# Performance work log

Hardware: AMD Instinct MI355X
Metric: run time of the kernel (lower is better)

## Reference

```python
import jax, jax.numpy as jnp
import numpy as np

BN_EPS = 1e-5
DIST_EPS = 1e-8


def setup_inputs() -> dict:
    key = jax.random.key(0)
    ks = jax.random.split(key, 8)
    B, N, S, D1, D2 = 8, 16384, 2048, 128, 256
    return {
        "xyz1": jax.random.normal(ks[0], (B, N, 3), jnp.float32),
        "xyz2": jax.random.normal(ks[1], (B, S, 3), jnp.float32),
        "points1": jax.random.normal(ks[2], (B, N, D1), jnp.float32),
        "points2": jax.random.normal(ks[3], (B, S, D2), jnp.float32),
        "w1": jax.random.normal(ks[4], (256, 384), jnp.float32) * 0.05,
        "b1": jnp.zeros((256,), jnp.float32),
        "g1": jnp.ones((256,), jnp.float32),
        "be1": jnp.zeros((256,), jnp.float32),
        "w2": jax.random.normal(ks[5], (128, 256), jnp.float32) * 0.05,
        "b2": jnp.zeros((128,), jnp.float32),
        "g2": jnp.ones((128,), jnp.float32),
        "be2": jnp.zeros((128,), jnp.float32),
        "fa1": jax.random.normal(ks[6], (16, 128), jnp.float32) * 0.1,
        "fa2": jax.random.normal(ks[7], (128, 16), jnp.float32) * 0.1,
    }


def _three_interp(xyz1, xyz2, points2):
    # squared pairwise distance [B,N,S]
    d = (jnp.sum(xyz1 ** 2, -1)[:, :, None]
         + jnp.sum(xyz2 ** 2, -1)[:, None, :]
         - 2.0 * jnp.einsum("bnc,bsc->bns", xyz1, xyz2))
    neg_d, idx = jax.lax.top_k(-d, 3)          # 3 smallest distances
    dist = -neg_d                               # [B,N,3]
    recip = 1.0 / (dist + DIST_EPS)
    w = recip / jnp.sum(recip, -1, keepdims=True)
    B, N, _ = idx.shape
    D = points2.shape[-1]
    gathered = jnp.take_along_axis(
        points2, idx.reshape(B, N * 3)[..., None], axis=1
    ).reshape(B, N, 3, D)
    return jnp.sum(gathered * w[..., None], axis=-2)  # [B,N,D]


def _bn_relu(h, g, be):
    # train-mode BatchNorm1d: stats over (batch, length)
    mu = jnp.mean(h, axis=(0, 1))
    var = jnp.var(h, axis=(0, 1))
    return jax.nn.relu(g * (h - mu) / jnp.sqrt(var + BN_EPS) + be)


def reference(xyz1, xyz2, points1, points2, w1, b1, g1, be1,
              w2, b2, g2, be2, fa1, fa2):
    interp = _three_interp(xyz1, xyz2, points2)          # [B,N,256]
    x = jnp.concatenate([points1, interp], axis=-1)      # [B,N,384]
    # 1x1 Conv1d + BN + ReLU stack (channel-last)
    x = _bn_relu(jnp.einsum("bnc,oc->bno", x, w1) + b1, g1, be1)  # [B,N,256]
    x = _bn_relu(jnp.einsum("bnc,oc->bno", x, w2) + b2, g2, be2)  # [B,N,128]
    # channel attention (SE-style, avg + max pool over length)
    def fc(v):  # v: [B,C]
        return jax.nn.relu(v @ fa1.T) @ fa2.T
    avg = jnp.mean(x, axis=1)
    mx = jnp.max(x, axis=1)
    scale = jax.nn.sigmoid(fc(avg) + fc(mx))             # [B,C]
    return x * scale[:, None, :]                          # [B,N,128]
```

## Files before the change

kernel.cpp:

```cpp
#include <hip/hip_runtime.h>
#include <math.h>

constexpr int BB = 8;
constexpr int NN = 16384;
constexpr int SS = 2048;
constexpr int D2 = 256;
constexpr int H1 = 256;
constexpr int H2 = 128;
constexpr int MM = BB * NN;
constexpr int LDB = 40;

typedef __attribute__((ext_vector_type(8))) short short8;
typedef __attribute__((ext_vector_type(16))) float f32x16;

__device__ __forceinline__ unsigned short f2b(float f) {
    union { float f; unsigned u; } v; v.f = f;
    unsigned r = v.u + 0x7FFFu + ((v.u >> 16) & 1u);
    return (unsigned short)(r >> 16);
}
__device__ __forceinline__ unsigned pk2(float lo, float hi) {
    return (unsigned)f2b(lo) | ((unsigned)f2b(hi) << 16);
}
__device__ __forceinline__ float b2f_lo(unsigned p) { return __uint_as_float(p << 16); }
__device__ __forceinline__ float b2f_hi(unsigned p) { return __uint_as_float(p & 0xFFFF0000u); }

__global__ void k_init(float* __restrict__ st1, float* __restrict__ st2,
                       float* __restrict__ psum, int* __restrict__ pmax) {
    int t = threadIdx.x;
    if (t < 512) st1[t] = 0.f;
    if (t < 256) st2[t] = 0.f;
    if (t < 1024) { psum[t] = 0.f; pmax[t] = 0; }
}

__global__ void k_wprep(const float* __restrict__ w1, const float* __restrict__ w2,
                        unsigned short* __restrict__ w1b, unsigned short* __restrict__ w2b) {
    int i = blockIdx.x * 256 + threadIdx.x;
    if (i < H1 * 384) w1b[i] = f2b(w1[i]);
    if (i < H2 * 256) w2b[i] = f2b(w2[i]);
}

__global__ void k_xyzprep(const float* __restrict__ xyz2, float4* __restrict__ xyz2p) {
    int i = blockIdx.x * 256 + threadIdx.x;
    if (i < BB * SS) {
        xyz2p[i] = make_float4(xyz2[i * 3], xyz2[i * 3 + 1], xyz2[i * 3 + 2], 0.f);
    }
}

__global__ __launch_bounds__(256) void k_knn(const float* __restrict__ xyz1,
                                             const float4* __restrict__ xyz2p,
                                             int* __restrict__ idx,
                                             float* __restrict__ wgt) {
    __shared__ unsigned cand[64][16];
    const int b = blockIdx.y;
    const int tid = threadIdx.x;
    const int ql = tid & 63;
    const int n = blockIdx.x * 64 + ql;

    const float* q = xyz1 + ((size_t)b * NN + n) * 3;
    const float qx = q[0], qy = q[1], qz = q[2];

    const int chunk = __builtin_amdgcn_readfirstlane(tid >> 6);
    const float4* cp = xyz2p + ((size_t)b << 11) + (chunk << 9);

    unsigned k0 = 0xFFFFFFFFu, k1 = 0xFFFFFFFFu, k2 = 0xFFFFFFFFu, k3 = 0xFFFFFFFFu;
#pragma unroll 4
    for (int j = 0; j < 512; ++j) {
        const float4 p = cp[j];
        const float dx = qx - p.x;
        const float dy = qy - p.y;
        const float dz = qz - p.z;
        const float d = fmaf(dx, dx, fmaf(dy, dy, dz * dz));
        const unsigned key = (__float_as_uint(d) & 0xFFFFFE00u) | (unsigned)j;
        unsigned m;
        m  = max(k0, key); k0 = min(k0, key);
        unsigned m2 = max(k1, m); k1 = min(k1, m);
        unsigned m3 = max(k2, m2); k2 = min(k2, m2);
        k3 = min(k3, m3);
    }
    unsigned* cq = cand[ql] + chunk * 4;
    cq[0] = k0; cq[1] = k1; cq[2] = k2; cq[3] = k3;
    __syncthreads();

    if (tid < 64) {
        const double qxd = (double)qx, qyd = (double)qy, qzd = (double)qz;
        double t0 = 1e300, t1 = 1e300, t2 = 1e300;
        int i0 = 0, i1 = 0, i2 = 0;
#pragma unroll
        for (int c = 0; c < 16; ++c) {
            const int s = ((c >> 2) << 9) + (int)(cand[tid][c] & 0x1FFu);
            const float4 p = xyz2p[((size_t)b << 11) + s];
            const double dx = qxd - (double)p.x;
            const double dy = qyd - (double)p.y;
            const double dz = qzd - (double)p.z;
            const double d = fma(dx, dx, fma(dy, dy, dz * dz));
            if (d < t2) {
                if (d < t0)      { t2 = t1; i2 = i1; t1 = t0; i1 = i0; t0 = d; i0 = s; }
                else if (d < t1) { t2 = t1; i2 = i1; t1 = d; i1 = s; }
                else             { t2 = d; i2 = s; }
            }
        }
        const double r0 = 1.0 / (t0 + 1e-8);
        const double r1 = 1.0 / (t1 + 1e-8);
        const double r2 = 1.0 / (t2 + 1e-8);
        const double inv = 1.0 / (r0 + r1 + r2);
        const size_t o = ((size_t)b * NN + n) * 3;
        idx[o + 0] = i0; idx[o + 1] = i1; idx[o + 2] = i2;
        wgt[o + 0] = (float)(r0 * inv);
        wgt[o + 1] = (float)(r1 * inv);
        wgt[o + 2] = (float)(r2 * inv);
    }
}

__global__ __launch_bounds__(256, 2) void k_gemm1(const float* __restrict__ p1,
                                                  const float* __restrict__ p2,
                                                  const int* __restrict__ idx,
                                                  const float* __restrict__ wgt,
                                                  const unsigned short* __restrict__ w1b,
                                                  const float* __restrict__ b1p,
                                                  unsigned short* __restrict__ h1b,
                                                  float* __restrict__ st1) {
    __shared__ __align__(16) unsigned short As[128 * LDB];
    __shared__ __align__(16) unsigned short Bs[256 * LDB];
    __shared__ float sSum[256], sSq[256];

    const int tid = threadIdx.x;
    const int row0 = blockIdx.x * 128;
    const int b = row0 >> 14;
    const float* p2b = p2 + (size_t)b * (SS * D2);

    sSum[tid] = 0.f; sSq[tid] = 0.f;

    const int wave = tid >> 6, lane = tid & 63;
    const int ln = lane & 31, hk = lane >> 5;
    const int wm = (wave & 1) << 6;
    const int wn = (wave >> 1) << 7;
    const int r = tid >> 1, half = tid & 1;

    const size_t o3 = (size_t)(row0 + r) * 3;
    const int j0 = idx[o3], j1 = idx[o3 + 1], j2 = idx[o3 + 2];
    const float wa = wgt[o3], wb = wgt[o3 + 1], wc = wgt[o3 + 2];
    const float* g0 = p2b + ((size_t)j0 << 8);
    const float* g1 = p2b + ((size_t)j1 << 8);
    const float* g2 = p2b + ((size_t)j2 << 8);

    f32x16 acc[2][4];
#pragma unroll
    for (int mt = 0; mt < 2; ++mt)
#pragma unroll
        for (int nt = 0; nt < 4; ++nt)
#pragma unroll
            for (int e = 0; e < 16; ++e) acc[mt][nt][e] = 0.f;

    float4 ra[12];
    uint4 rb[4];

    auto prefetch = [&](int kc) {
        const unsigned short* bsrc = w1b + (size_t)tid * 384 + kc * 32;
        rb[0] = *(const uint4*)(bsrc);
        rb[1] = *(const uint4*)(bsrc + 8);
        rb[2] = *(const uint4*)(bsrc + 16);
        rb[3] = *(const uint4*)(bsrc + 24);
        if (kc < 4) {
            const float* src = p1 + (((size_t)(row0 + r)) << 7) + kc * 32 + half * 16;
            ra[0] = *(const float4*)(src);
            ra[1] = *(const float4*)(src + 4);
            ra[2] = *(const float4*)(src + 8);
            ra[3] = *(const float4*)(src + 12);
        } else {
            const int c2 = kc * 32 - 128 + half * 16;
#pragma unroll
            for (int g = 0; g < 4; ++g) {
                ra[g]     = *(const float4*)(g0 + c2 + g * 4);
                ra[4 + g] = *(const float4*)(g1 + c2 + g * 4);
                ra[8 + g] = *(const float4*)(g2 + c2 + g * 4);
            }
        }
    };

    prefetch(0);

    for (int kc = 0; kc < 12; ++kc) {
        uint4 pa0, pa1;
        if (kc < 4) {
            pa0 = make_uint4(pk2(ra[0].x, ra[0].y), pk2(ra[0].z, ra[0].w),
                             pk2(ra[1].x, ra[1].y), pk2(ra[1].z, ra[1].w));
            pa1 = make_uint4(pk2(ra[2].x, ra[2].y), pk2(ra[2].z, ra[2].w),
                             pk2(ra[3].x, ra[3].y), pk2(ra[3].z, ra[3].w));
        } else {
            float v[16];
#pragma unroll
            for (int g = 0; g < 4; ++g) {
                v[g * 4 + 0] = fmaf(wa, ra[g].x, fmaf(wb, ra[4 + g].x, wc * ra[8 + g].x));
                v[g * 4 + 1] = fmaf(wa, ra[g].y, fmaf(wb, ra[4 + g].y, wc * ra[8 + g].y));
                v[g * 4 + 2] = fmaf(wa, ra[g].z, fmaf(wb, ra[4 + g].z, wc * ra[8 + g].z));
                v[g * 4 + 3] = fmaf(wa, ra[g].w, fmaf(wb, ra[4 + g].w, wc * ra[8 + g].w));
            }
            pa0 = make_uint4(pk2(v[0], v[1]), pk2(v[2], v[3]), pk2(v[4], v[5]), pk2(v[6], v[7]));
            pa1 = make_uint4(pk2(v[8], v[9]), pk2(v[10], v[11]), pk2(v[12], v[13]), pk2(v[14], v[15]));
        }
        const uint4 wb0 = rb[0], wb1 = rb[1], wb2 = rb[2], wb3 = rb[3];

        __syncthreads();
        *(uint4*)&As[r * LDB + half * 16] = pa0;
        *(uint4*)&As[r * LDB + half * 16 + 8] = pa1;
        *(uint4*)&Bs[tid * LDB + 0]  = wb0;
        *(uint4*)&Bs[tid * LDB + 8]  = wb1;
        *(uint4*)&Bs[tid * LDB + 16] = wb2;
        *(uint4*)&Bs[tid * LDB + 24] = wb3;
        __syncthreads();

        if (kc < 11) prefetch(kc + 1);

        short8 af[2][2], bfv[4][2];
#pragma unroll
        for (int mt = 0; mt < 2; ++mt)
#pragma unroll
            for (int ks = 0; ks < 2; ++ks)
                af[mt][ks] = *(const short8*)&As[(wm + mt * 32 + ln) * LDB + ks * 16 + hk * 8];
#pragma unroll
        for (int nt = 0; nt < 4; ++nt)
#pragma unroll
            for (int ks = 0; ks < 2; ++ks)
                bfv[nt][ks] = *(const short8*)&Bs[(wn + nt * 32 + ln) * LDB + ks * 16 + hk * 8];
#pragma unroll
        for (int mt = 0; mt < 2; ++mt)
#pragma unroll
            for (int nt = 0; nt < 4; ++nt)
#pragma unroll
                for (int ks = 0; ks < 2; ++ks)
                    acc[mt][nt] = __builtin_amdgcn_mfma_f32_32x32x16_bf16(
                        af[mt][ks], bfv[nt][ks], acc[mt][nt], 0, 0, 0);
    }

#pragma unroll
    for (int nt = 0; nt < 4; ++nt) {
        const int col = wn + nt * 32 + ln;
        const float bias = b1p[col];
        float ps = 0.f, pq = 0.f;
#pragma unroll
        for (int mt = 0; mt < 2; ++mt) {
#pragma unroll
            for (int e = 0; e < 16; ++e) {
                const int rl = wm + mt * 32 + (e & 3) + ((e >> 2) << 3) + (hk << 2);
                const float o = acc[mt][nt][e] + bias;
                ps += o;
                pq = fmaf(o, o, pq);
                h1b[(((size_t)(row0 + rl)) << 8) + col] = f2b(o);
            }
        }
        atomicAdd(&sSum[col], ps);
        atomicAdd(&sSq[col], pq);
    }
    __syncthreads();
    atomicAdd(&st1[tid], sSum[tid]);
    atomicAdd(&st1[256 + tid], sSq[tid]);
}

__global__ void k_bnprep(const float* __restrict__ st, const float* __restrict__ g,
                         const float* __restrict__ be, float* __restrict__ bn,
                         int C, float invM) {
    int c = blockIdx.x * blockDim.x + threadIdx.x;
    if (c < C) {
        float mean = st[c] * invM;
        float var = st[C + c] * invM - mean * mean;
        float a = g[c] / sqrtf(var + 1e-5f);
        bn[c] = a;
        bn[C + c] = fmaf(-mean, a, be[c]);
    }
}

__global__ __launch_bounds__(256) void k_gemm2(const unsigned short* __restrict__ h1b,
                                               const unsigned short* __restrict__ w2b,
                                               const float* __restrict__ b2p,
                                               const float* __restrict__ bn1,
                                               unsigned short* __restrict__ h2b,
                                               float* __restrict__ st2) {
    __shared__ __align__(16) unsigned short As[128 * LDB];
    __shared__ __align__(16) unsigned short Bs[128 * LDB];
    __shared__ float sBNa[256], sBNb[256];
    __shared__ float sSum[128], sSq[128];

    const int tid = threadIdx.x;
    const int row0 = blockIdx.x * 128;

    sBNa[tid] = bn1[tid];
    sBNb[tid] = bn1[256 + tid];
    if (tid < 128) { sSum[tid] = 0.f; sSq[tid] = 0.f; }

    const int wave = tid >> 6, lane = tid & 63;
    const int ln = lane & 31, hk = lane >> 5;
    const int wm = (wave & 1) << 6, wn = (wave >> 1) << 6;
    const int r = tid >> 1, half = tid & 1;

    f32x16 acc[2][2];
#pragma unroll
    for (int mt = 0; mt < 2; ++mt)
#pragma unroll
        for (int nt = 0; nt < 2; ++nt)
#pragma unroll
            for (int e = 0; e < 16; ++e) acc[mt][nt][e] = 0.f;

    uint4 rA0, rA1, rB0, rB1;
    auto prefetch = [&](int kc) {
        const unsigned short* asrc = h1b + (size_t)(row0 + r) * 256 + kc * 32 + half * 16;
        rA0 = *(const uint4*)asrc;
        rA1 = *(const uint4*)(asrc + 8);
        const unsigned short* bsrc = w2b + (size_t)r * 256 + kc * 32 + half * 16;
        rB0 = *(const uint4*)bsrc;
        rB1 = *(const uint4*)(bsrc + 8);
    };

    prefetch(0);
    __syncthreads();

    for (int kc = 0; kc < 8; ++kc) {
        const int k0 = kc * 32 + half * 16;
        unsigned pw[8] = {rA0.x, rA0.y, rA0.z, rA0.w, rA1.x, rA1.y, rA1.z, rA1.w};
        unsigned po[8];
#pragma unroll
        for (int gi = 0; gi < 8; ++gi) {
            float lo = b2f_lo(pw[gi]);
            float hi = b2f_hi(pw[gi]);
            lo = fmaxf(fmaf(sBNa[k0 + 2 * gi], lo, sBNb[k0 + 2 * gi]), 0.f);
            hi = fmaxf(fmaf(sBNa[k0 + 2 * gi + 1], hi, sBNb[k0 + 2 * gi + 1]), 0.f);
            po[gi] = pk2(lo, hi);
        }
        const uint4 pa0 = make_uint4(po[0], po[1], po[2], po[3]);
        const uint4 pa1 = make_uint4(po[4], po[5], po[6], po[7]);
        const uint4 qb0 = rB0, qb1 = rB1;

        __syncthreads();
        *(uint4*)&As[r * LDB + half * 16] = pa0;
        *(uint4*)&As[r * LDB + half * 16 + 8] = pa1;
        *(uint4*)&Bs[r * LDB + half * 16] = qb0;
        *(uint4*)&Bs[r * LDB + half * 16 + 8] = qb1;
        __syncthreads();

        if (kc < 7) prefetch(kc + 1);

        short8 af[2][2], bfv[2][2];
#pragma unroll
        for (int mt = 0; mt < 2; ++mt)
#pragma unroll
            for (int ks = 0; ks < 2; ++ks)
                af[mt][ks] = *(const short8*)&As[(wm + mt * 32 + ln) * LDB + ks * 16 + hk * 8];
#pragma unroll
        for (int nt = 0; nt < 2; ++nt)
#pragma unroll
            for (int ks = 0; ks < 2; ++ks)
                bfv[nt][ks] = *(const short8*)&Bs[(wn + nt * 32 + ln) * LDB + ks * 16 + hk * 8];
#pragma unroll
        for (int mt = 0; mt < 2; ++mt)
#pragma unroll
            for (int nt = 0; nt < 2; ++nt)
#pragma unroll
                for (int ks = 0; ks < 2; ++ks)
                    acc[mt][nt] = __builtin_amdgcn_mfma_f32_32x32x16_bf16(
                        af[mt][ks], bfv[nt][ks], acc[mt][nt], 0, 0, 0);
    }

#pragma unroll
    for (int nt = 0; nt < 2; ++nt) {
        const int col = wn + nt * 32 + ln;
        const float bias = b2p[col];
        float ps = 0.f, pq = 0.f;
#pragma unroll
        for (int mt = 0; mt < 2; ++mt) {
#pragma unroll
            for (int e = 0; e < 16; ++e) {
                const int rl = wm + mt * 32 + (e & 3) + ((e >> 2) << 3) + (hk << 2);
                const float o = acc[mt][nt][e] + bias;
                ps += o;
                pq = fmaf(o, o, pq);
                h2b[(((size_t)(row0 + rl)) << 7) + col] = f2b(o);
            }
        }
        atomicAdd(&sSum[col], ps);
        atomicAdd(&sSq[col], pq);
    }
    __syncthreads();
    if (tid < 128) {
        atomicAdd(&st2[tid], sSum[tid]);
        atomicAdd(&st2[128 + tid], sSq[tid]);
    }
}

__global__ __launch_bounds__(256) void k_pool(const unsigned short* __restrict__ h2b,
                                              const float* __restrict__ bn2,
                                              float* __restrict__ psum,
                                              int* __restrict__ pmax) {
    const int b = blockIdx.y;
    const int n0 = blockIdx.x * 256;
    const int tid = threadIdx.x;
    const int c = tid & 127, rh = tid >> 7;
    const float a = bn2[c], bc = bn2[128 + c];
    const unsigned short* base = h2b + (((size_t)b * NN + n0 + rh) << 7) + c;
    float s = 0.f, m = 0.f;
    for (int i = 0; i < 128; ++i) {
        float v = __uint_as_float((unsigned)base[(size_t)i * 256] << 16);
        float x = fmaxf(fmaf(a, v, bc), 0.f);
        s += x;
        m = fmaxf(m, x);
    }
    __shared__ float rs[256];
    __shared__ float rm[256];
    rs[tid] = s; rm[tid] = m;
    __syncthreads();
    if (tid < 128) {
        float ts = rs[tid] + rs[tid + 128];
        float tm = fmaxf(rm[tid], rm[tid + 128]);
        atomicAdd(&psum[b * 128 + c], ts);
        atomicMax(&pmax[b * 128 + c], __float_as_int(tm));
    }
}

__global__ __launch_bounds__(1024) void k_attn(const float* __restrict__ psum,
                                               const int* __restrict__ pmax,
                                               const float* __restrict__ fa1,
                                               const float* __restrict__ fa2,
                                               const float* __restrict__ bn2,
                                               float* __restrict__ sa,
                                               float* __restrict__ sb) {
    __shared__ float tS[128];
    const int tid = threadIdx.x;
    if (tid < 128) {
        const int b = tid >> 4, j = tid & 15;
        float da = 0.f, dm = 0.f;
        for (int cc = 0; cc < 128; ++cc) {
            float f = fa1[j * 128 + cc];
            da = fmaf(psum[b * 128 + cc] * (1.0f / 16384.0f), f, da);
            dm = fmaf(__int_as_float(pmax[b * 128 + cc]), f, dm);
        }
        tS[tid] = fmaxf(da, 0.f) + fmaxf(dm, 0.f);
    }
    __syncthreads();
    const int b = tid >> 7, c = tid & 127;
    float s = 0.f;
#pragma unroll
    for (int j = 0; j < 16; ++j) s = fmaf(tS[b * 16 + j], fa2[c * 16 + j], s);
    const float sc = 1.f / (1.f + expf(-s));
    sa[b * 128 + c] = bn2[c] * sc;
    sb[b * 128 + c] = bn2[128 + c] * sc;
}

__global__ void k_final(const unsigned short* __restrict__ h2b, const float* __restrict__ sa,
                        const float* __restrict__ sb, float* __restrict__ out) {
    const size_t i = (size_t)blockIdx.x * blockDim.x + threadIdx.x;
    const int cg = (int)(i & 15) * 8;
    const size_t row = i >> 4;
    const int b = (int)(row >> 14);
    const uint4 h = *(const uint4*)(h2b + (row << 7) + cg);
    const float4 A0 = *(const float4*)&sa[b * 128 + cg];
    const float4 A1 = *(const float4*)&sa[b * 128 + cg + 4];
    const float4 B0 = *(const float4*)&sb[b * 128 + cg];
    const float4 B1 = *(const float4*)&sb[b * 128 + cg + 4];
    float4 o0, o1;
    o0.x = fmaxf(fmaf(A0.x, b2f_lo(h.x), B0.x), 0.f);
    o0.y = fmaxf(fmaf(A0.y, b2f_hi(h.x), B0.y), 0.f);
    o0.z = fmaxf(fmaf(A0.z, b2f_lo(h.y), B0.z), 0.f);
    o0.w = fmaxf(fmaf(A0.w, b2f_hi(h.y), B0.w), 0.f);
    o1.x = fmaxf(fmaf(A1.x, b2f_lo(h.z), B1.x), 0.f);
    o1.y = fmaxf(fmaf(A1.y, b2f_hi(h.z), B1.y), 0.f);
    o1.z = fmaxf(fmaf(A1.z, b2f_lo(h.w), B1.z), 0.f);
    o1.w = fmaxf(fmaf(A1.w, b2f_hi(h.w), B1.w), 0.f);
    *(float4*)(out + (row << 7) + cg) = o0;
    *(float4*)(out + (row << 7) + cg + 4) = o1;
}

extern "C" void kernel_launch(void* const* d_in, const int* in_sizes, int n_in,
                              void* d_out, int out_size, void* d_ws, size_t ws_size,
                              hipStream_t stream) {
    const float* xyz1 = (const float*)d_in[0];
    const float* xyz2 = (const float*)d_in[1];
    const float* p1   = (const float*)d_in[2];
    const float* p2   = (const float*)d_in[3];
    const float* w1   = (const float*)d_in[4];
    const float* b1   = (const float*)d_in[5];
    const float* g1   = (const float*)d_in[6];
    const float* be1  = (const float*)d_in[7];
    const float* w2   = (const float*)d_in[8];
    const float* b2   = (const float*)d_in[9];
    const float* g2   = (const float*)d_in[10];
    const float* be2  = (const float*)d_in[11];
    const float* fa1  = (const float*)d_in[12];
    const float* fa2  = (const float*)d_in[13];
    float* out = (float*)d_out;

    char* ws = (char*)d_ws;
    int*   idx  = (int*)ws;
    float* wgt  = (float*)(ws + 1572864);
    unsigned short* h1b = (unsigned short*)(ws + 3145728);
    unsigned short* h2b = (unsigned short*)(ws + 70254592);
    float* st1  = (float*)(ws + 103809024);
    float* bn1  = st1 + 512;
    float* st2  = bn1 + 512;
    float* bn2  = st2 + 256;
    float* psum = bn2 + 256;
    int*   pmax = (int*)(psum + 1024);
    float* sa   = (float*)(pmax + 1024);
    float* sb   = sa + 1024;
    unsigned short* w1b = (unsigned short*)(sb + 1024);
    unsigned short* w2b = w1b + 98304;
    float4* xyz2p = (float4*)(ws + 104857600);

    k_init<<<1, 1024, 0, stream>>>(st1, st2, psum, pmax);
    k_wprep<<<(H1 * 384 + 255) / 256, 256, 0, stream>>>(w1, w2, w1b, w2b);
    k_xyzprep<<<(BB * SS + 255) / 256, 256, 0, stream>>>(xyz2, xyz2p);
    k_knn<<<dim3(NN / 64, BB), 256, 0, stream>>>(xyz1, xyz2p, idx, wgt);
    k_gemm1<<<MM / 128, 256, 0, stream>>>(p1, p2, idx, wgt, w1b, b1, h1b, st1);
    k_bnprep<<<1, 256, 0, stream>>>(st1, g1, be1, bn1, 256, 1.0f / (float)MM);
    k_gemm2<<<MM / 128, 256, 0, stream>>>(h1b, w2b, b2, bn1, h2b, st2);
    k_bnprep<<<1, 128, 0, stream>>>(st2, g2, be2, bn2, 128, 1.0f / (float)MM);
    k_pool<<<dim3(NN / 256, BB), 256, 0, stream>>>(h2b, bn2, psum, pmax);
    k_attn<<<1, 1024, 0, stream>>>(psum, pmax, fa1, fa2, bn2, sa, sb);
    k_final<<<(MM * H2 / 8) / 256, 256, 0, stream>>>(h2b, sa, sb, out);
}
```

Before: 413.9 us.

## Precompute points2 projection through W1 and interpolate projected features

Since the interpolation is linear, the points2 part of the first conv is computed once per source point (Z = points2·W1[:,128:]) in a new small GEMM kernel. The main GEMM then covers only the 128 points1 channels and adds a weighted gather of three Z rows in its epilogue. This cuts the interpolated GEMM work and gather traffic roughly by the N/S ratio. In exchange, the epilogue does scattered fp32 gathers from an 16 MB Z buffer that reuses the h2b workspace. Tiles shrink to 64 rows so occupancy is raised to 3 blocks.

```diff
diff --git a/kernel.cpp b/kernel.cpp
--- a/kernel.cpp
+++ b/kernel.cpp
@@ -111,146 +111,204 @@
     }
 }
 
-__global__ __launch_bounds__(256, 2) void k_gemm1(const float* __restrict__ p1,
-                                                  const float* __restrict__ p2,
+__global__ __launch_bounds__(256) void k_zprep(const float* __restrict__ p2,
+                                               const unsigned short* __restrict__ w1b,
+                                               float* __restrict__ Z) {
+    __shared__ __align__(16) unsigned short As[64 * LDB];
+    __shared__ __align__(16) unsigned short Bs[256 * LDB];
+    const int tid = threadIdx.x;
+    const int s0 = blockIdx.x * 64;
+    const int wave = tid >> 6, lane = tid & 63;
+    const int ln = lane & 31, hk = lane >> 5;
+    const int wn = wave << 6;
+    const int r = tid >> 2, q = tid & 3;
+
+    f32x16 acc[2][2];
+#pragma unroll
+    for (int mt = 0; mt < 2; ++mt)
+#pragma unroll
+        for (int nt = 0; nt < 2; ++nt)
+#pragma unroll
+            for (int e = 0; e < 16; ++e) acc[mt][nt][e] = 0.f;
+
+    float4 ra[2];
+    uint4 rb[4];
+    auto prefetch = [&](int kc) {
+        const unsigned short* bsrc = w1b + (size_t)tid * 384 + 128 + kc * 32;
+        rb[0] = *(const uint4*)(bsrc);
+        rb[1] = *(const uint4*)(bsrc + 8);
+        rb[2] = *(const uint4*)(bsrc + 16);
+        rb[3] = *(const uint4*)(bsrc + 24);
+        const float* asrc = p2 + (((size_t)(s0 + r)) << 8) + kc * 32 + q * 8;
+        ra[0] = *(const float4*)(asrc);
+        ra[1] = *(const float4*)(asrc + 4);
+    };
+
+    prefetch(0);
+
+    for (int kc = 0; kc < 8; ++kc) {
+        const uint4 pa = make_uint4(pk2(ra[0].x, ra[0].y), pk2(ra[0].z, ra[0].w),
+                                    pk2(ra[1].x, ra[1].y), pk2(ra[1].z, ra[1].w));
+        const uint4 b0 = rb[0], b1 = rb[1], b2 = rb[2], b3 = rb[3];
+
+        __syncthreads();
+        *(uint4*)&As[r * LDB + q * 8] = pa;
+        *(uint4*)&Bs[tid * LDB + 0]  = b0;
+        *(uint4*)&Bs[tid * LDB + 8]  = b1;
+        *(uint4*)&Bs[tid * LDB + 16] = b2;
+        *(uint4*)&Bs[tid * LDB + 24] = b3;
+        __syncthreads();
+
+        if (kc < 7) prefetch(kc + 1);
+
+        short8 af[2][2], bfv[2][2];
+#pragma unroll
+        for (int mt = 0; mt < 2; ++mt)
+#pragma unroll
+            for (int ks = 0; ks < 2; ++ks)
+                af[mt][ks] = *(const short8*)&As[(mt * 32 + ln) * LDB + ks * 16 + hk * 8];
+#pragma unroll
+        for (int nt = 0; nt < 2; ++nt)
+#pragma unroll
+            for (int ks = 0; ks < 2; ++ks)
+                bfv[nt][ks] = *(const short8*)&Bs[(wn + nt * 32 + ln) * LDB + ks * 16 + hk * 8];
+#pragma unroll
+        for (int mt = 0; mt < 2; ++mt)
+#pragma unroll
+            for (int nt = 0; nt < 2; ++nt)
+#pragma unroll
+                for (int ks = 0; ks < 2; ++ks)
+                    acc[mt][nt] = __builtin_amdgcn_mfma_f32_32x32x16_bf16(
+                        af[mt][ks], bfv[nt][ks], acc[mt][nt], 0, 0, 0);
+    }
+
+#pragma unroll
+    for (int mt = 0; mt < 2; ++mt)
+#pragma unroll
+        for (int nt = 0; nt < 2; ++nt)
+#pragma unroll
+            for (int e = 0; e < 16; ++e) {
+                const int rl = mt * 32 + (e & 3) + ((e >> 2) << 3) + (hk << 2);
+                Z[(((size_t)(s0 + rl)) << 8) + wn + nt * 32 + ln] = acc[mt][nt][e];
+            }
+}
+
+__global__ __launch_bounds__(256, 3) void k_gemm1(const float* __restrict__ p1,
                                                   const int* __restrict__ idx,
                                                   const float* __restrict__ wgt,
                                                   const unsigned short* __restrict__ w1b,
                                                   const float* __restrict__ b1p,
+                                                  const float* __restrict__ Z,
                                                   unsigned short* __restrict__ h1b,
                                                   float* __restrict__ st1) {
-    __shared__ __align__(16) unsigned short As[128 * LDB];
+    __shared__ __align__(16) unsigned short As[64 * LDB];
     __shared__ __align__(16) unsigned short Bs[256 * LDB];
     __shared__ float sSum[256], sSq[256];
+    __shared__ int   sJ[64][3];
+    __shared__ float sW[64][3];
 
     const int tid = threadIdx.x;
-    const int row0 = blockIdx.x * 128;
+    const int row0 = blockIdx.x * 64;
     const int b = row0 >> 14;
-    const float* p2b = p2 + (size_t)b * (SS * D2);
 
     sSum[tid] = 0.f; sSq[tid] = 0.f;
+    if (tid < 64) {
+        const size_t o3 = (size_t)(row0 + tid) * 3;
+        sJ[tid][0] = idx[o3]; sJ[tid][1] = idx[o3 + 1]; sJ[tid][2] = idx[o3 + 2];
+        sW[tid][0] = wgt[o3]; sW[tid][1] = wgt[o3 + 1]; sW[tid][2] = wgt[o3 + 2];
+    }
 
     const int wave = tid >> 6, lane = tid & 63;
     const int ln = lane & 31, hk = lane >> 5;
-    const int wm = (wave & 1) << 6;
-    const int wn = (wave >> 1) << 7;
-    const int r = tid >> 1, half = tid & 1;
-
-    const size_t o3 = (size_t)(row0 + r) * 3;
-    const int j0 = idx[o3], j1 = idx[o3 + 1], j2 = idx[o3 + 2];
-    const float wa = wgt[o3], wb = wgt[o3 + 1], wc = wgt[o3 + 2];
-    const float* g0 = p2b + ((size_t)j0 << 8);
-    const float* g1 = p2b + ((size_t)j1 << 8);
-    const float* g2 = p2b + ((size_t)j2 << 8);
-
-    f32x16 acc[2][4];
+    const int wn = wave << 6;
+    const int r = tid >> 2, q = tid & 3;
+
+    f32x16 acc[2][2];
 #pragma unroll
     for (int mt = 0; mt < 2; ++mt)
 #pragma unroll
-        for (int nt = 0; nt < 4; ++nt)
+        for (int nt = 0; nt < 2; ++nt)
 #pragma unroll
             for (int e = 0; e < 16; ++e) acc[mt][nt][e] = 0.f;
 
-    float4 ra[12];
+    float4 ra[2];
     uint4 rb[4];
-
     auto prefetch = [&](int kc) {
         const unsigned short* bsrc = w1b + (size_t)tid * 384 + kc * 32;
         rb[0] = *(const uint4*)(bsrc);
         rb[1] = *(const uint4*)(bsrc + 8);
         rb[2] = *(const uint4*)(bsrc + 16);
         rb[3] = *(const uint4*)(bsrc + 24);
-        if (kc < 4) {
-            const float* src = p1 + (((size_t)(row0 + r)) << 7) + kc * 32 + half * 16;
-            ra[0] = *(const float4*)(src);
-            ra[1] = *(const float4*)(src + 4);
-            ra[2] = *(const float4*)(src + 8);
-            ra[3] = *(const float4*)(src + 12);
-        } else {
-            const int c2 = kc * 32 - 128 + half * 16;
-#pragma unroll
-            for (int g = 0; g < 4; ++g) {
-                ra[g]     = *(const float4*)(g0 + c2 + g * 4);
-                ra[4 + g] = *(const float4*)(g1 + c2 + g * 4);
-                ra[8 + g] = *(const float4*)(g2 + c2 + g * 4);
-            }
-        }
+        const float* asrc = p1 + (((size_t)(row0 + r)) << 7) + kc * 32 + q * 8;
+        ra[0] = *(const float4*)(asrc);
+        ra[1] = *(const float4*)(asrc + 4);
     };
 
     prefetch(0);
 
-    for (int kc = 0; kc < 12; ++kc) {
-        uint4 pa0, pa1;
-        if (kc < 4) {
-            pa0 = make_uint4(pk2(ra[0].x, ra[0].y), pk2(ra[0].z, ra[0].w),
-                             pk2(ra[1].x, ra[1].y), pk2(ra[1].z, ra[1].w));
-            pa1 = make_uint4(pk2(ra[2].x, ra[2].y), pk2(ra[2].z, ra[2].w),
-                             pk2(ra[3].x, ra[3].y), pk2(ra[3].z, ra[3].w));
-        } else {
-            float v[16];
-#pragma unroll
-            for (int g = 0; g < 4; ++g) {
-                v[g * 4 + 0] = fmaf(wa, ra[g].x, fmaf(wb, ra[4 + g].x, wc * ra[8 + g].x));
-                v[g * 4 + 1] = fmaf(wa, ra[g].y, fmaf(wb, ra[4 + g].y, wc * ra[8 + g].y));
-                v[g * 4 + 2] = fmaf(wa, ra[g].z, fmaf(wb, ra[4 + g].z, wc * ra[8 + g].z));
-                v[g * 4 + 3] = fmaf(wa, ra[g].w, fmaf(wb, ra[4 + g].w, wc * ra[8 + g].w));
-            }
-            pa0 = make_uint4(pk2(v[0], v[1]), pk2(v[2], v[3]), pk2(v[4], v[5]), pk2(v[6], v[7]));
-            pa1 = make_uint4(pk2(v[8], v[9]), pk2(v[10], v[11]), pk2(v[12], v[13]), pk2(v[14], v[15]));
-        }
-        const uint4 wb0 = rb[0], wb1 = rb[1], wb2 = rb[2], wb3 = rb[3];
+    for (int kc = 0; kc < 4; ++kc) {
+        const uint4 pa = make_uint4(pk2(ra[0].x, ra[0].y), pk2(ra[0].z, ra[0].w),
+                                    pk2(ra[1].x, ra[1].y), pk2(ra[1].z, ra[1].w));
+        const uint4 b0 = rb[0], b1 = rb[1], b2 = rb[2], b3 = rb[3];
 
         __syncthreads();
-        *(uint4*)&As[r * LDB + half * 16] = pa0;
-        *(uint4*)&As[r * LDB + half * 16 + 8] = pa1;
-        *(uint4*)&Bs[tid * LDB + 0]  = wb0;
-        *(uint4*)&Bs[tid * LDB + 8]  = wb1;
-        *(uint4*)&Bs[tid * LDB + 16] = wb2;
-        *(uint4*)&Bs[tid * LDB + 24] = wb3;
+        *(uint4*)&As[r * LDB + q * 8] = pa;
+        *(uint4*)&Bs[tid * LDB + 0]  = b0;
+        *(uint4*)&Bs[tid * LDB + 8]  = b1;
+        *(uint4*)&Bs[tid * LDB + 16] = b2;
+        *(uint4*)&Bs[tid * LDB + 24] = b3;
         __syncthreads();
 
-        if (kc < 11) prefetch(kc + 1);
-
-        short8 af[2][2], bfv[4][2];
+        if (kc < 3) prefetch(kc + 1);
+
+        short8 af[2][2], bfv[2][2];
 #pragma unroll
         for (int mt = 0; mt < 2; ++mt)
 #pragma unroll
             for (int ks = 0; ks < 2; ++ks)
-                af[mt][ks] = *(const short8*)&As[(wm + mt * 32 + ln) * LDB + ks * 16 + hk * 8];
-#pragma unroll
-        for (int nt = 0; nt < 4; ++nt)
+                af[mt][ks] = *(const short8*)&As[(mt * 32 + ln) * LDB + ks * 16 + hk * 8];
+#pragma unroll
+        for (int nt = 0; nt < 2; ++nt)
 #pragma unroll
             for (int ks = 0; ks < 2; ++ks)
                 bfv[nt][ks] = *(const short8*)&Bs[(wn + nt * 32 + ln) * LDB + ks * 16 + hk * 8];
 #pragma unroll
         for (int mt = 0; mt < 2; ++mt)
 #pragma unroll
-            for (int nt = 0; nt < 4; ++nt)
+            for (int nt = 0; nt < 2; ++nt)
 #pragma unroll
                 for (int ks = 0; ks < 2; ++ks)
                     acc[mt][nt] = __builtin_amdgcn_mfma_f32_32x32x16_bf16(
                         af[mt][ks], bfv[nt][ks], acc[mt][nt], 0, 0, 0);
     }
 
-#pragma unroll
-    for (int nt = 0; nt < 4; ++nt) {
-        const int col = wn + nt * 32 + ln;
-        const float bias = b1p[col];
-        float ps = 0.f, pq = 0.f;
-#pragma unroll
-        for (int mt = 0; mt < 2; ++mt) {
-#pragma unroll
-            for (int e = 0; e < 16; ++e) {
-                const int rl = wm + mt * 32 + (e & 3) + ((e >> 2) << 3) + (hk << 2);
-                const float o = acc[mt][nt][e] + bias;
-                ps += o;
-                pq = fmaf(o, o, pq);
-                h1b[(((size_t)(row0 + rl)) << 8) + col] = f2b(o);
-            }
+    const float* Zb = Z + ((size_t)b << 19);
+    const int c0 = wn + ln;
+    const float bias0 = b1p[c0];
+    const float bias1 = b1p[c0 + 32];
+    float ps0 = 0.f, pq0 = 0.f, ps1 = 0.f, pq1 = 0.f;
+#pragma unroll
+    for (int mt = 0; mt < 2; ++mt) {
+#pragma unroll
+        for (int e = 0; e < 16; ++e) {
+            const int rl = mt * 32 + (e & 3) + ((e >> 2) << 3) + (hk << 2);
+            const float* z0 = Zb + (((size_t)sJ[rl][0]) << 8) + c0;
+            const float* z1 = Zb + (((size_t)sJ[rl][1]) << 8) + c0;
+            const float* z2 = Zb + (((size_t)sJ[rl][2]) << 8) + c0;
+            const float wa = sW[rl][0], wb2 = sW[rl][1], wc = sW[rl][2];
+            const float v0 = fmaf(wa, z0[0],  fmaf(wb2, z1[0],  wc * z2[0]));
+            const float v1 = fmaf(wa, z0[32], fmaf(wb2, z1[32], wc * z2[32]));
+            const float o0 = acc[mt][0][e] + bias0 + v0;
+            const float o1 = acc[mt][1][e] + bias1 + v1;
+            ps0 += o0; pq0 = fmaf(o0, o0, pq0);
+            ps1 += o1; pq1 = fmaf(o1, o1, pq1);
+            const size_t ro = ((size_t)(row0 + rl)) << 8;
+            h1b[ro + c0]      = f2b(o0);
+            h1b[ro + c0 + 32] = f2b(o1);
         }
-        atomicAdd(&sSum[col], ps);
-        atomicAdd(&sSq[col], pq);
-    }
+    }
+    atomicAdd(&sSum[c0], ps0);      atomicAdd(&sSq[c0], pq0);
+    atomicAdd(&sSum[c0 + 32], ps1); atomicAdd(&sSq[c0 + 32], pq1);
     __syncthreads();
     atomicAdd(&st1[tid], sSum[tid]);
     atomicAdd(&st1[256 + tid], sSq[tid]);
@@ -491,6 +549,7 @@
     float* wgt  = (float*)(ws + 1572864);
     unsigned short* h1b = (unsigned short*)(ws + 3145728);
     unsigned short* h2b = (unsigned short*)(ws + 70254592);
+    float* Zbuf = (float*)(ws + 70254592);
     float* st1  = (float*)(ws + 103809024);
     float* bn1  = st1 + 512;
     float* st2  = bn1 + 512;
@@ -506,8 +565,9 @@
     k_init<<<1, 1024, 0, stream>>>(st1, st2, psum, pmax);
     k_wprep<<<(H1 * 384 + 255) / 256, 256, 0, stream>>>(w1, w2, w1b, w2b);
     k_xyzprep<<<(BB * SS + 255) / 256, 256, 0, stream>>>(xyz2, xyz2p);
+    k_zprep<<<BB * SS / 64, 256, 0, stream>>>(p2, w1b, Zbuf);
     k_knn<<<dim3(NN / 64, BB), 256, 0, stream>>>(xyz1, xyz2p, idx, wgt);
-    k_gemm1<<<MM / 128, 256, 0, stream>>>(p1, p2, idx, wgt, w1b, b1, h1b, st1);
+    k_gemm1<<<MM / 64, 256, 0, stream>>>(p1, idx, wgt, w1b, b1, Zbuf, h1b, st1);
     k_bnprep<<<1, 256, 0, stream>>>(st1, g1, be1, bn1, 256, 1.0f / (float)MM);
     k_gemm2<<<MM / 128, 256, 0, stream>>>(h1b, w2b, b2, bn1, h2b, st2);
     k_bnprep<<<1, 128, 0, stream>>>(st2, g2, be2, bn2, 128, 1.0f / (float)MM);
```

Result: no change. 420.0 us (+1.5%).
